# Kernel optimization log

Measured on AMD Instinct MI355X. Metric: run time of the kernel, lower is better.

Reference implementation:

```python
import jax, jax.numpy as jnp
import numpy as np

EPS = 1e-5

def _block(x, W, b, g, be):
    # Linear -> LayerNorm -> ReLU, fused elementwise chain
    h = x @ W + b
    mu = jnp.mean(h, axis=-1, keepdims=True)
    var = jnp.mean(jnp.square(h - mu), axis=-1, keepdims=True)
    hn = (h - mu) * jax.lax.rsqrt(var + EPS) * g + be
    return jnp.maximum(hn, 0.0)

def setup_inputs() -> dict:
    key = jax.random.key(0)
    ks = jax.random.split(key, 6)
    B, D_IN, H, D_OUT = 262144, 48, 256, 12
    s_in = 1.0 / np.sqrt(D_IN)
    s_h = 1.0 / np.sqrt(H)
    return {
        "x": jax.random.normal(ks[0], (B, D_IN), jnp.float32),
        "W1": jax.random.normal(ks[1], (D_IN, H), jnp.float32) * s_in,
        "b1": jnp.zeros((H,), jnp.float32),
        "g1": jnp.ones((H,), jnp.float32),
        "be1": jnp.zeros((H,), jnp.float32),
        "W2": jax.random.normal(ks[2], (H, H), jnp.float32) * s_h,
        "b2": jnp.zeros((H,), jnp.float32),
        "g2": jnp.ones((H,), jnp.float32),
        "be2": jnp.zeros((H,), jnp.float32),
        "W3": jax.random.normal(ks[3], (H, H), jnp.float32) * s_h,
        "b3": jnp.zeros((H,), jnp.float32),
        "g3": jnp.ones((H,), jnp.float32),
        "be3": jnp.zeros((H,), jnp.float32),
        "Wm": jax.random.normal(ks[4], (H, D_OUT), jnp.float32) * s_h,
        "bm": jnp.zeros((D_OUT,), jnp.float32),
    }

def reference(x, W1, b1, g1, be1, W2, b2, g2, be2, W3, b3, g3, be3, Wm, bm):
    h = _block(x, W1, b1, g1, be1)
    h = _block(h, W2, b2, g2, be2)
    h = _block(h, W3, b3, g3, be3)
    return jnp.tanh(h @ Wm + bm)
```

## Files before the change

### kernel.cpp

```cpp
#include <hip/hip_runtime.h>
#include <hip/hip_bf16.h>

#define BATCH 262144
#define DIN 48
#define HDIM 256
#define DOUT 12
#define EPSV 1e-5f

#define ROWS_PER_BLOCK 128
#define NBLK (BATCH / ROWS_PER_BLOCK)

typedef __attribute__((ext_vector_type(4))) float f32x4;
typedef __attribute__((ext_vector_type(8))) short bf16x8;

union FragU { bf16x8 v; unsigned u[4]; };

#define W1F_OFF 0
#define W2F_OFF 16384
#define W3F_OFF 81920
#define WMF_OFF 147456
#define WS_ELEMS 151552

__device__ __forceinline__ unsigned short f2b(float f) {
    union { float f; unsigned u; } v; v.f = f;
    unsigned r = (v.u + 0x7fffu + ((v.u >> 16) & 1u)) >> 16;
    return (unsigned short)r;
}

__device__ __forceinline__ unsigned packbf(float a, float b) {
    float2 t; t.x = a; t.y = b;
    __hip_bfloat162 h = __float22bfloat162_rn(t);
    union { __hip_bfloat162 h; unsigned u; } c; c.h = h;
    return c.u;
}

__device__ __forceinline__ float fast_tanh(float x) {
    const float t = __expf(2.0f * x);
    return fmaf(-2.0f, __builtin_amdgcn_rcpf(t + 1.0f), 1.0f);
}

__global__ void conv_w_kernel(const float* __restrict__ W1, const float* __restrict__ b1,
                              const float* __restrict__ W2, const float* __restrict__ W3,
                              const float* __restrict__ Wm,
                              unsigned short* __restrict__ ws) {
    int i = blockIdx.x * 256 + threadIdx.x;
    if (i >= WS_ELEMS) return;
    float v;
    if (i < W2F_OFF) {
        const int j = i & 7, l = (i >> 3) & 63, t = (i >> 9) & 15, s = i >> 13;
        const int n = 16 * t + (l & 15), k = 32 * s + 8 * (l >> 4) + j;
        v = (k < DIN) ? W1[k * HDIM + n] : (k == DIN ? b1[n] : 0.0f);
    } else if (i < W3F_OFF) {
        const int i2 = i - W2F_OFF;
        const int j = i2 & 7, l = (i2 >> 3) & 63, t = (i2 >> 9) & 15, s = i2 >> 13;
        const int n = 16 * t + (l & 15);
        const int k = 32 * s + ((j >= 4) ? 16 : 0) + 4 * (l >> 4) + (j & 3);
        v = W2[k * HDIM + n];
    } else if (i < WMF_OFF) {
        const int i3 = i - W3F_OFF;
        const int j = i3 & 7, l = (i3 >> 3) & 63, t = (i3 >> 9) & 15, s = i3 >> 13;
        const int n = 16 * t + (l & 15);
        const int k = 32 * s + ((j >= 4) ? 16 : 0) + 4 * (l >> 4) + (j & 3);
        v = W3[k * HDIM + n];
    } else {
        const int i4 = i - WMF_OFF;
        const int j = i4 & 7, l = (i4 >> 3) & 63, ks = i4 >> 9;
        const int n = l & 15;
        const int k = 32 * ks + ((j >= 4) ? 16 : 0) + 4 * (l >> 4) + (j & 3);
        v = (n < DOUT) ? Wm[k * DOUT + n] : 0.0f;
    }
    ws[i] = f2b(v);
}

__device__ __forceinline__ void gll16(const void* g, void* l) {
    __builtin_amdgcn_global_load_lds(
        (const __attribute__((address_space(1))) unsigned int*)g,
        (__attribute__((address_space(3))) unsigned int*)l, 16, 0, 0);
}

__device__ __forceinline__ void stage_pair(const unsigned short* __restrict__ src,
                                           unsigned short* dst, int tid) {
    const char* g = (const char*)src + tid * 16;
    char* l = (char*)dst + tid * 16;
    #pragma unroll
    for (int c = 0; c < 8; c++)
        gll16(g + c * 4096, l + c * 4096);
}

template<int NP>
__device__ __forceinline__ void mm_layer(
    f32x4 (&acc)[2][16], const FragU (&bf)[2][8],
    unsigned short (&buf)[2][16384], int& p,
    const unsigned short* __restrict__ wt, const unsigned short* __restrict__ wtnext,
    int tid, int lane)
{
    #pragma unroll
    for (int pp = 0; pp < NP; pp++) {
        const unsigned short* nxt = (pp + 1 < NP) ? (wt + (pp + 1) * 16384) : wtnext;
        if (nxt) stage_pair(nxt, &buf[p ^ 1][0], tid);
        __builtin_amdgcn_s_setprio(1);
        #pragma unroll
        for (int h = 0; h < 2; h++) {
            #pragma unroll
            for (int t = 0; t < 16; t++) {
                const bf16x8 A = *(const bf16x8*)&buf[p][h * 8192 + (t * 64 + lane) * 8];
                acc[0][t] = __builtin_amdgcn_mfma_f32_16x16x32_bf16(A, bf[0][2 * pp + h].v, acc[0][t], 0, 0, 0);
                acc[1][t] = __builtin_amdgcn_mfma_f32_16x16x32_bf16(A, bf[1][2 * pp + h].v, acc[1][t], 0, 0, 0);
            }
        }
        __builtin_amdgcn_s_setprio(0);
        __syncthreads();
        p ^= 1;
    }
}

__device__ __forceinline__ void build_frags(
    const f32x4 (&acc)[2][16], FragU (&bfo)[2][8],
    const float2* __restrict__ gbeL, int lane)
{
    const int q = lane >> 4;
    #pragma unroll
    for (int rt = 0; rt < 2; rt++) {
        float ss = 0.f, qq = 0.f;
        #pragma unroll
        for (int t = 0; t < 16; t++)
            #pragma unroll
            for (int r = 0; r < 4; r++) {
                const float v = acc[rt][t][r];
                ss += v; qq = fmaf(v, v, qq);
            }
        ss += __shfl_xor(ss, 16); ss += __shfl_xor(ss, 32);
        qq += __shfl_xor(qq, 16); qq += __shfl_xor(qq, 32);
        const float mu = ss * (1.0f / 256.0f);
        const float rs = __builtin_amdgcn_rsqf(
            fmaxf(qq * (1.0f / 256.0f) - mu * mu, 0.0f) + EPSV);
        const float nb = -mu * rs;
        #pragma unroll
        for (int ks = 0; ks < 8; ks++) {
            const float4 a0 = *(const float4*)&gbeL[32 * ks + 4 * q];
            const float4 a1 = *(const float4*)&gbeL[32 * ks + 4 * q + 2];
            const float4 b0 = *(const float4*)&gbeL[32 * ks + 16 + 4 * q];
            const float4 b1 = *(const float4*)&gbeL[32 * ks + 16 + 4 * q + 2];
            float w00 = fmaxf(fmaf(fmaf(acc[rt][2 * ks][0], rs, nb), a0.x, a0.y), 0.f);
            float w01 = fmaxf(fmaf(fmaf(acc[rt][2 * ks][1], rs, nb), a0.z, a0.w), 0.f);
            float w02 = fmaxf(fmaf(fmaf(acc[rt][2 * ks][2], rs, nb), a1.x, a1.y), 0.f);
            float w03 = fmaxf(fmaf(fmaf(acc[rt][2 * ks][3], rs, nb), a1.z, a1.w), 0.f);
            float w10 = fmaxf(fmaf(fmaf(acc[rt][2 * ks + 1][0], rs, nb), b0.x, b0.y), 0.f);
            float w11 = fmaxf(fmaf(fmaf(acc[rt][2 * ks + 1][1], rs, nb), b0.z, b0.w), 0.f);
            float w12 = fmaxf(fmaf(fmaf(acc[rt][2 * ks + 1][2], rs, nb), b1.x, b1.y), 0.f);
            float w13 = fmaxf(fmaf(fmaf(acc[rt][2 * ks + 1][3], rs, nb), b1.z, b1.w), 0.f);
            bfo[rt][ks].u[0] = packbf(w00, w01);
            bfo[rt][ks].u[1] = packbf(w02, w03);
            bfo[rt][ks].u[2] = packbf(w10, w11);
            bfo[rt][ks].u[3] = packbf(w12, w13);
        }
    }
}

__device__ __forceinline__ void zero_acc(f32x4 (&acc)[2][16]) {
    #pragma unroll
    for (int rt = 0; rt < 2; rt++)
        #pragma unroll
        for (int t = 0; t < 16; t++)
            acc[rt][t] = (f32x4){0.f, 0.f, 0.f, 0.f};
}

__device__ __forceinline__ void init_acc_bias(f32x4 (&acc)[2][16],
                                              const float* __restrict__ bt, int q) {
    #pragma unroll
    for (int t = 0; t < 16; t++) {
        const float4 b = *(const float4*)&bt[16 * t + 4 * q];
        acc[0][t] = (f32x4){b.x, b.y, b.z, b.w};
        acc[1][t] = (f32x4){b.x, b.y, b.z, b.w};
    }
}

__global__ __launch_bounds__(256, 2) void fused_mlp(
    const float* __restrict__ x,
    const float* __restrict__ g1, const float* __restrict__ be1,
    const float* __restrict__ b2, const float* __restrict__ g2, const float* __restrict__ be2,
    const float* __restrict__ b3, const float* __restrict__ g3, const float* __restrict__ be3,
    const float* __restrict__ bm,
    const unsigned short* __restrict__ ws,
    float* __restrict__ out)
{
    __shared__ unsigned short buf[2][16384];
    __shared__ float2 gbe[3][256];
    __shared__ float btab[2][256];
    __shared__ float bmt[16];
    __shared__ float ostage[4][384];

    const int tid = threadIdx.x;
    const int wv = tid >> 6, lane = tid & 63;
    const int l15 = lane & 15, q = lane >> 4;
    const int wrow0 = blockIdx.x * ROWS_PER_BLOCK + wv * 32;

    const unsigned short* w1f = ws + W1F_OFF;
    const unsigned short* w2f = ws + W2F_OFF;
    const unsigned short* w3f = ws + W3F_OFF;
    const unsigned short* wmf = ws + WMF_OFF;

    stage_pair(w1f, &buf[0][0], tid);
    {
        const int n = tid;
        gbe[0][n] = make_float2(g1[n], be1[n]);
        gbe[1][n] = make_float2(g2[n], be2[n]);
        gbe[2][n] = make_float2(g3[n], be3[n]);
        btab[0][n] = b2[n];
        btab[1][n] = b3[n];
        if (tid < 16) bmt[tid] = (tid < DOUT) ? bm[tid] : 0.f;
    }
    FragU bf[2][8];
    #pragma unroll
    for (int rt = 0; rt < 2; rt++) {
        const float* xr = x + (size_t)(wrow0 + rt * 16 + l15) * DIN;
        const float4 f0 = *(const float4*)(xr + q * 8);
        const float4 f1 = *(const float4*)(xr + q * 8 + 4);
        bf[rt][0].u[0] = packbf(f0.x, f0.y); bf[rt][0].u[1] = packbf(f0.z, f0.w);
        bf[rt][0].u[2] = packbf(f1.x, f1.y); bf[rt][0].u[3] = packbf(f1.z, f1.w);
        if (q < 2) {
            const float4 f2 = *(const float4*)(xr + 32 + q * 8);
            const float4 f3 = *(const float4*)(xr + 36 + q * 8);
            bf[rt][1].u[0] = packbf(f2.x, f2.y); bf[rt][1].u[1] = packbf(f2.z, f2.w);
            bf[rt][1].u[2] = packbf(f3.x, f3.y); bf[rt][1].u[3] = packbf(f3.z, f3.w);
        } else if (q == 2) {
            bf[rt][1].u[0] = 0x00003F80u;
            bf[rt][1].u[1] = 0u; bf[rt][1].u[2] = 0u; bf[rt][1].u[3] = 0u;
        } else {
            bf[rt][1].u[0] = 0u; bf[rt][1].u[1] = 0u;
            bf[rt][1].u[2] = 0u; bf[rt][1].u[3] = 0u;
        }
    }
    __syncthreads();

    f32x4 acc[2][16];
    int p = 0;

    zero_acc(acc);
    mm_layer<1>(acc, bf, buf, p, w1f, w2f, tid, lane);
    build_frags(acc, bf, &gbe[0][0], lane);

    init_acc_bias(acc, &btab[0][0], q);
    mm_layer<4>(acc, bf, buf, p, w2f, w3f, tid, lane);
    build_frags(acc, bf, &gbe[1][0], lane);

    init_acc_bias(acc, &btab[1][0], q);
    mm_layer<4>(acc, bf, buf, p, w3f, (const unsigned short*)nullptr, tid, lane);
    build_frags(acc, bf, &gbe[2][0], lane);

    f32x4 facc[2];
    {
        const float4 bm4 = *(const float4*)&bmt[4 * q];
        facc[0] = (f32x4){bm4.x, bm4.y, bm4.z, bm4.w};
        facc[1] = facc[0];
    }
    #pragma unroll
    for (int ks = 0; ks < 8; ks++) {
        const bf16x8 A = *(const bf16x8*)&wmf[(ks * 64 + lane) * 8];
        facc[0] = __builtin_amdgcn_mfma_f32_16x16x32_bf16(A, bf[0][ks].v, facc[0], 0, 0, 0);
        facc[1] = __builtin_amdgcn_mfma_f32_16x16x32_bf16(A, bf[1][ks].v, facc[1], 0, 0, 0);
    }
    if (q < 3) {
        #pragma unroll
        for (int rt = 0; rt < 2; rt++) {
            float4 o;
            o.x = fast_tanh(facc[rt][0]);
            o.y = fast_tanh(facc[rt][1]);
            o.z = fast_tanh(facc[rt][2]);
            o.w = fast_tanh(facc[rt][3]);
            *(float4*)&ostage[wv][(rt * 16 + l15) * 12 + q * 4] = o;
        }
    }
    float4* og = (float4*)(out + (size_t)wrow0 * DOUT);
    const float4* ov = (const float4*)&ostage[wv][0];
    og[lane] = ov[lane];
    if (lane < 32) og[64 + lane] = ov[64 + lane];
}

extern "C" void kernel_launch(void* const* d_in, const int* in_sizes, int n_in,
                              void* d_out, int out_size, void* d_ws, size_t ws_size,
                              hipStream_t stream)
{
    const float* x   = (const float*)d_in[0];
    const float* W1  = (const float*)d_in[1];
    const float* b1  = (const float*)d_in[2];
    const float* g1  = (const float*)d_in[3];
    const float* be1 = (const float*)d_in[4];
    const float* W2  = (const float*)d_in[5];
    const float* b2  = (const float*)d_in[6];
    const float* g2  = (const float*)d_in[7];
    const float* be2 = (const float*)d_in[8];
    const float* W3  = (const float*)d_in[9];
    const float* b3  = (const float*)d_in[10];
    const float* g3  = (const float*)d_in[11];
    const float* be3 = (const float*)d_in[12];
    const float* Wm  = (const float*)d_in[13];
    const float* bm  = (const float*)d_in[14];
    unsigned short* ws = (unsigned short*)d_ws;
    float* out = (float*)d_out;

    conv_w_kernel<<<(WS_ELEMS + 255) / 256, 256, 0, stream>>>(W1, b1, W2, W3, Wm, ws);
    fused_mlp<<<NBLK, 256, 0, stream>>>(x, g1, be1, b2, g2, be2,
                                        b3, g3, be3, bm, ws, out);
}
```

Baseline: 103.0 us.

## Pipeline weight staging as a four-slab ring with vmcnt waits and packed LN math

Weight staging now uses a four-slot ring of half-size slabs with two slabs of prefetch in flight. Explicit s_waitcnt vmcnt counts plus raw s_barrier replace the per-pair __syncthreads, and the prefetch stream carries across layer boundaries. The goal is to keep global-to-LDS loads overlapped with MFMA work and to cut full-drain synchronisation. The LayerNorm/ReLU fragment build is rewritten with packed float2 vector math, using separate gamma and beta tables, to encourage packed FMA. The hand-counted vmcnt values tie correctness to the exact number of outstanding loads, which is a fragile dependency.

```diff
diff --git a/kernel.cpp b/kernel.cpp
--- a/kernel.cpp
+++ b/kernel.cpp
@@ -11,6 +11,7 @@
 #define NBLK (BATCH / ROWS_PER_BLOCK)
 
 typedef __attribute__((ext_vector_type(4))) float f32x4;
+typedef __attribute__((ext_vector_type(2))) float f32x2;
 typedef __attribute__((ext_vector_type(8))) short bf16x8;
 
 union FragU { bf16x8 v; unsigned u[4]; };
@@ -20,6 +21,8 @@
 #define W3F_OFF 81920
 #define WMF_OFF 147456
 #define WS_ELEMS 151552
+
+#define WAITV(n) asm volatile("s_waitcnt vmcnt(" #n ")" ::: "memory")
 
 __device__ __forceinline__ unsigned short f2b(float f) {
     union { float f; unsigned u; } v; v.f = f;
@@ -78,81 +81,77 @@
         (__attribute__((address_space(3))) unsigned int*)l, 16, 0, 0);
 }
 
-__device__ __forceinline__ void stage_pair(const unsigned short* __restrict__ src,
+__device__ __forceinline__ void stage_slab(const unsigned short* __restrict__ src,
                                            unsigned short* dst, int tid) {
     const char* g = (const char*)src + tid * 16;
     char* l = (char*)dst + tid * 16;
     #pragma unroll
-    for (int c = 0; c < 8; c++)
+    for (int c = 0; c < 4; c++)
         gll16(g + c * 4096, l + c * 4096);
 }
 
-template<int NP>
-__device__ __forceinline__ void mm_layer(
-    f32x4 (&acc)[2][16], const FragU (&bf)[2][8],
-    unsigned short (&buf)[2][16384], int& p,
-    const unsigned short* __restrict__ wt, const unsigned short* __restrict__ wtnext,
-    int tid, int lane)
+__device__ __forceinline__ void compute_slab(
+    f32x4 (&acc)[2][16], const FragU& b0, const FragU& b1,
+    const unsigned short* sb, int lane)
 {
-    #pragma unroll
-    for (int pp = 0; pp < NP; pp++) {
-        const unsigned short* nxt = (pp + 1 < NP) ? (wt + (pp + 1) * 16384) : wtnext;
-        if (nxt) stage_pair(nxt, &buf[p ^ 1][0], tid);
-        __builtin_amdgcn_s_setprio(1);
-        #pragma unroll
-        for (int h = 0; h < 2; h++) {
-            #pragma unroll
-            for (int t = 0; t < 16; t++) {
-                const bf16x8 A = *(const bf16x8*)&buf[p][h * 8192 + (t * 64 + lane) * 8];
-                acc[0][t] = __builtin_amdgcn_mfma_f32_16x16x32_bf16(A, bf[0][2 * pp + h].v, acc[0][t], 0, 0, 0);
-                acc[1][t] = __builtin_amdgcn_mfma_f32_16x16x32_bf16(A, bf[1][2 * pp + h].v, acc[1][t], 0, 0, 0);
-            }
-        }
-        __builtin_amdgcn_s_setprio(0);
-        __syncthreads();
-        p ^= 1;
-    }
-}
+    __builtin_amdgcn_s_setprio(1);
+    #pragma unroll
+    for (int t = 0; t < 16; t++) {
+        const bf16x8 A = *(const bf16x8*)&sb[(t * 64 + lane) * 8];
+        acc[0][t] = __builtin_amdgcn_mfma_f32_16x16x32_bf16(A, b0.v, acc[0][t], 0, 0, 0);
+        acc[1][t] = __builtin_amdgcn_mfma_f32_16x16x32_bf16(A, b1.v, acc[1][t], 0, 0, 0);
+    }
+    __builtin_amdgcn_s_setprio(0);
+}
+
+#define SV2(v, a, b) __builtin_shufflevector(v, v, a, b)
 
 __device__ __forceinline__ void build_frags(
     const f32x4 (&acc)[2][16], FragU (&bfo)[2][8],
-    const float2* __restrict__ gbeL, int lane)
+    const float* __restrict__ gt, const float* __restrict__ bt, int lane)
 {
-    const int q = lane >> 4;
+    const int q4 = (lane >> 4) * 4;
     #pragma unroll
     for (int rt = 0; rt < 2; rt++) {
-        float ss = 0.f, qq = 0.f;
+        f32x2 s2 = {0.f, 0.f}, p2 = {0.f, 0.f};
         #pragma unroll
-        for (int t = 0; t < 16; t++)
-            #pragma unroll
-            for (int r = 0; r < 4; r++) {
-                const float v = acc[rt][t][r];
-                ss += v; qq = fmaf(v, v, qq);
-            }
+        for (int t = 0; t < 16; t++) {
+            const f32x2 a = SV2(acc[rt][t], 0, 1);
+            const f32x2 b = SV2(acc[rt][t], 2, 3);
+            s2 += a; s2 += b;
+            p2 += a * a; p2 += b * b;
+        }
+        float ss = s2[0] + s2[1];
+        float qq = p2[0] + p2[1];
         ss += __shfl_xor(ss, 16); ss += __shfl_xor(ss, 32);
         qq += __shfl_xor(qq, 16); qq += __shfl_xor(qq, 32);
         const float mu = ss * (1.0f / 256.0f);
         const float rs = __builtin_amdgcn_rsqf(
             fmaxf(qq * (1.0f / 256.0f) - mu * mu, 0.0f) + EPSV);
         const float nb = -mu * rs;
+        const f32x2 rs2 = {rs, rs}, nb2 = {nb, nb}, z2 = {0.f, 0.f};
         #pragma unroll
         for (int ks = 0; ks < 8; ks++) {
-            const float4 a0 = *(const float4*)&gbeL[32 * ks + 4 * q];
-            const float4 a1 = *(const float4*)&gbeL[32 * ks + 4 * q + 2];
-            const float4 b0 = *(const float4*)&gbeL[32 * ks + 16 + 4 * q];
-            const float4 b1 = *(const float4*)&gbeL[32 * ks + 16 + 4 * q + 2];
-            float w00 = fmaxf(fmaf(fmaf(acc[rt][2 * ks][0], rs, nb), a0.x, a0.y), 0.f);
-            float w01 = fmaxf(fmaf(fmaf(acc[rt][2 * ks][1], rs, nb), a0.z, a0.w), 0.f);
-            float w02 = fmaxf(fmaf(fmaf(acc[rt][2 * ks][2], rs, nb), a1.x, a1.y), 0.f);
-            float w03 = fmaxf(fmaf(fmaf(acc[rt][2 * ks][3], rs, nb), a1.z, a1.w), 0.f);
-            float w10 = fmaxf(fmaf(fmaf(acc[rt][2 * ks + 1][0], rs, nb), b0.x, b0.y), 0.f);
-            float w11 = fmaxf(fmaf(fmaf(acc[rt][2 * ks + 1][1], rs, nb), b0.z, b0.w), 0.f);
-            float w12 = fmaxf(fmaf(fmaf(acc[rt][2 * ks + 1][2], rs, nb), b1.x, b1.y), 0.f);
-            float w13 = fmaxf(fmaf(fmaf(acc[rt][2 * ks + 1][3], rs, nb), b1.z, b1.w), 0.f);
-            bfo[rt][ks].u[0] = packbf(w00, w01);
-            bfo[rt][ks].u[1] = packbf(w02, w03);
-            bfo[rt][ks].u[2] = packbf(w10, w11);
-            bfo[rt][ks].u[3] = packbf(w12, w13);
+            const f32x4 g0 = *(const f32x4*)&gt[32 * ks + q4];
+            const f32x4 e0 = *(const f32x4*)&bt[32 * ks + q4];
+            const f32x4 g1 = *(const f32x4*)&gt[32 * ks + 16 + q4];
+            const f32x4 e1 = *(const f32x4*)&bt[32 * ks + 16 + q4];
+            const f32x2 v00 = SV2(acc[rt][2 * ks], 0, 1);
+            const f32x2 v01 = SV2(acc[rt][2 * ks], 2, 3);
+            const f32x2 v10 = SV2(acc[rt][2 * ks + 1], 0, 1);
+            const f32x2 v11 = SV2(acc[rt][2 * ks + 1], 2, 3);
+            const f32x2 w00 = __builtin_elementwise_max(
+                (v00 * rs2 + nb2) * SV2(g0, 0, 1) + SV2(e0, 0, 1), z2);
+            const f32x2 w01 = __builtin_elementwise_max(
+                (v01 * rs2 + nb2) * SV2(g0, 2, 3) + SV2(e0, 2, 3), z2);
+            const f32x2 w10 = __builtin_elementwise_max(
+                (v10 * rs2 + nb2) * SV2(g1, 0, 1) + SV2(e1, 0, 1), z2);
+            const f32x2 w11 = __builtin_elementwise_max(
+                (v11 * rs2 + nb2) * SV2(g1, 2, 3) + SV2(e1, 2, 3), z2);
+            bfo[rt][ks].u[0] = packbf(w00[0], w00[1]);
+            bfo[rt][ks].u[1] = packbf(w01[0], w01[1]);
+            bfo[rt][ks].u[2] = packbf(w10[0], w10[1]);
+            bfo[rt][ks].u[3] = packbf(w11[0], w11[1]);
         }
     }
 }
@@ -169,9 +168,9 @@
                                               const float* __restrict__ bt, int q) {
     #pragma unroll
     for (int t = 0; t < 16; t++) {
-        const float4 b = *(const float4*)&bt[16 * t + 4 * q];
-        acc[0][t] = (f32x4){b.x, b.y, b.z, b.w};
-        acc[1][t] = (f32x4){b.x, b.y, b.z, b.w};
+        const f32x4 b = *(const f32x4*)&bt[16 * t + 4 * q];
+        acc[0][t] = b;
+        acc[1][t] = b;
     }
 }
 
@@ -184,8 +183,9 @@
     const unsigned short* __restrict__ ws,
     float* __restrict__ out)
 {
-    __shared__ unsigned short buf[2][16384];
-    __shared__ float2 gbe[3][256];
+    __shared__ unsigned short buf[4][8192];
+    __shared__ float gtab[3][256];
+    __shared__ float betab[3][256];
     __shared__ float btab[2][256];
     __shared__ float bmt[16];
     __shared__ float ostage[4][384];
@@ -200,12 +200,14 @@
     const unsigned short* w3f = ws + W3F_OFF;
     const unsigned short* wmf = ws + WMF_OFF;
 
-    stage_pair(w1f, &buf[0][0], tid);
+    stage_slab(w1f, &buf[0][0], tid);
+    stage_slab(w1f + 8192, &buf[1][0], tid);
+
     {
         const int n = tid;
-        gbe[0][n] = make_float2(g1[n], be1[n]);
-        gbe[1][n] = make_float2(g2[n], be2[n]);
-        gbe[2][n] = make_float2(g3[n], be3[n]);
+        gtab[0][n] = g1[n];  betab[0][n] = be1[n];
+        gtab[1][n] = g2[n];  betab[1][n] = be2[n];
+        gtab[2][n] = g3[n];  betab[2][n] = be3[n];
         btab[0][n] = b2[n];
         btab[1][n] = b3[n];
         if (tid < 16) bmt[tid] = (tid < DOUT) ? bm[tid] : 0.f;
@@ -231,28 +233,53 @@
             bf[rt][1].u[2] = 0u; bf[rt][1].u[3] = 0u;
         }
     }
-    __syncthreads();
+    asm volatile("s_waitcnt lgkmcnt(0)" ::: "memory");
 
     f32x4 acc[2][16];
-    int p = 0;
+
 
     zero_acc(acc);
-    mm_layer<1>(acc, bf, buf, p, w1f, w2f, tid, lane);
-    build_frags(acc, bf, &gbe[0][0], lane);
+    #pragma unroll
+    for (int s = 0; s < 2; s++) {
+        stage_slab(w2f + s * 8192, &buf[(s + 2) & 3][0], tid);
+        WAITV(8);
+        __builtin_amdgcn_s_barrier();
+        __builtin_amdgcn_sched_barrier(0);
+        compute_slab(acc, bf[0][s], bf[1][s], &buf[s][0], lane);
+    }
+    build_frags(acc, bf, &gtab[0][0], &betab[0][0], lane);
 
     init_acc_bias(acc, &btab[0][0], q);
-    mm_layer<4>(acc, bf, buf, p, w2f, w3f, tid, lane);
-    build_frags(acc, bf, &gbe[1][0], lane);
+    #pragma unroll
+    for (int s = 0; s < 8; s++) {
+        const unsigned short* nsrc = (s < 6) ? (w2f + (s + 2) * 8192)
+                                             : (w3f + (s - 6) * 8192);
+        stage_slab(nsrc, &buf[(s + 4) & 3][0], tid);
+        WAITV(8);
+        __builtin_amdgcn_s_barrier();
+        __builtin_amdgcn_sched_barrier(0);
+        compute_slab(acc, bf[0][s], bf[1][s], &buf[(s + 2) & 3][0], lane);
+    }
+    build_frags(acc, bf, &gtab[1][0], &betab[1][0], lane);
 
     init_acc_bias(acc, &btab[1][0], q);
-    mm_layer<4>(acc, bf, buf, p, w3f, (const unsigned short*)nullptr, tid, lane);
-    build_frags(acc, bf, &gbe[2][0], lane);
+    #pragma unroll
+    for (int s = 0; s < 8; s++) {
+        if (s < 6) stage_slab(w3f + (s + 2) * 8192, &buf[(s + 12) & 3][0], tid);
+        if (s < 6)      { WAITV(8); }
+        else if (s == 6){ WAITV(4); }
+        else            { WAITV(0); }
+        __builtin_amdgcn_s_barrier();
+        __builtin_amdgcn_sched_barrier(0);
+        compute_slab(acc, bf[0][s], bf[1][s], &buf[(s + 10) & 3][0], lane);
+    }
+    build_frags(acc, bf, &gtab[2][0], &betab[2][0], lane);
 
     f32x4 facc[2];
     {
-        const float4 bm4 = *(const float4*)&bmt[4 * q];
-        facc[0] = (f32x4){bm4.x, bm4.y, bm4.z, bm4.w};
-        facc[1] = facc[0];
+        const f32x4 bm4 = *(const f32x4*)&bmt[4 * q];
+        facc[0] = bm4;
+        facc[1] = bm4;
     }
     #pragma unroll
     for (int ks = 0; ks < 8; ks++) {
```

New measurement: 100.6 us, median of 2. 2.4% less time.
